# Optimization experiments

Measured on AMD Instinct MI355X. Metric: run time of the kernel, lower is better.

Reference implementation:

```python
import jax, jax.numpy as jnp
import numpy as np

B, S, E = 2, 4096, 640
H, D, G = 4, 256, 1      # n_heads, head_dim, n_kv_groups
WINDOW = 512
SCALING = 256.0 ** -0.5  # query_pre_attn_scalar ** -0.5
EPS = 1e-6


def rmsnorm(x, scale):
    # Gemma variant: weight = 1 + scale, computed in fp32 over last dim
    xf = x.astype(jnp.float32)
    var = jnp.mean(xf * xf, axis=-1, keepdims=True)
    return (xf * jax.lax.rsqrt(var + EPS) * (1.0 + scale.astype(jnp.float32))).astype(x.dtype)


def apply_rope(x, cos, sin):
    # x: [B, h, S, D]; cos/sin: [S, D]
    half = x.shape[-1] // 2
    x1, x2 = x[..., :half], x[..., half:]
    rotated = jnp.concatenate([-x2, x1], axis=-1)
    return (x * cos[None, None] + rotated * sin[None, None]).astype(x.dtype)


def setup_inputs() -> dict:
    key = jax.random.key(0)
    ks = jax.random.split(key, 6)
    x = jax.random.normal(ks[0], (B, S, E), dtype=jnp.float32)
    # weights (torch Linear weight.T layout: [in, out])
    Wq = jax.random.normal(ks[1], (E, H * D), dtype=jnp.float32) * 0.02
    Wk = jax.random.normal(ks[2], (E, G * D), dtype=jnp.float32) * 0.02
    Wv = jax.random.normal(ks[3], (E, G * D), dtype=jnp.float32) * 0.02
    Wo = jax.random.normal(ks[4], (H * D, E), dtype=jnp.float32) * 0.02
    q_scale = jnp.zeros((D,), dtype=jnp.float32)
    k_scale = jnp.zeros((D,), dtype=jnp.float32)
    # RoPE tables (theta = rope_local_base = 10000 for sliding layers)
    inv_freq = 1.0 / (10000.0 ** (jnp.arange(0, D, 2, dtype=jnp.float32) / D))
    angles = jnp.arange(S, dtype=jnp.float32)[:, None] * inv_freq[None, :]
    angles = jnp.concatenate([angles, angles], axis=1)  # [S, D]
    cos, sin = jnp.cos(angles), jnp.sin(angles)
    # causal + sliding-window mask; True = masked out
    i = jnp.arange(S)[:, None]
    j = jnp.arange(S)[None, :]
    mask = (j > i) | ((i - j) >= WINDOW)
    return {"x": x, "mask": mask, "cos": cos, "sin": sin,
            "Wq": Wq, "Wk": Wk, "Wv": Wv, "Wo": Wo,
            "q_scale": q_scale, "k_scale": k_scale}


def reference(x, mask, cos, sin, Wq, Wk, Wv, Wo, q_scale, k_scale):
    b, s, _ = x.shape
    q = (x @ Wq).reshape(b, s, H, D).transpose(0, 2, 1, 3)  # [B,H,S,D]
    k = (x @ Wk).reshape(b, s, G, D).transpose(0, 2, 1, 3)  # [B,G,S,D]
    v = (x @ Wv).reshape(b, s, G, D).transpose(0, 2, 1, 3)  # [B,G,S,D]
    q = rmsnorm(q, q_scale)
    k = rmsnorm(k, k_scale)
    q = apply_rope(q, cos, sin)
    k = apply_rope(k, cos, sin)
    # GQA: K/V have G=1 heads; broadcasting replaces repeat_interleave
    scores = (q * SCALING) @ jnp.swapaxes(k, -1, -2)  # [B,H,S,S]
    scores = jnp.where(mask[None, None], -jnp.inf, scores)
    attn = jax.nn.softmax(scores, axis=-1)
    out = attn @ v                                     # [B,H,S,D]
    out = out.transpose(0, 2, 1, 3).reshape(b, s, H * D)
    return out @ Wo
```

## Files before the change

kernel.cpp:

```cpp
#include <hip/hip_runtime.h>
#include <hip/hip_bf16.h>
#include <stdint.h>

#define BB 2
#define SS 4096
#define EE 640
#define HH 4
#define DD 256
#define WIN 512

typedef __attribute__((ext_vector_type(8))) short bv8;
typedef __attribute__((ext_vector_type(4))) float fv4;
typedef __attribute__((ext_vector_type(16))) float fv16;

__device__ __forceinline__ unsigned short f2b(float f) {
  union { float f; unsigned u; } a; a.f = f;
  unsigned r = a.u + 0x7fffu + ((a.u >> 16) & 1u);
  return (unsigned short)(r >> 16);
}
__device__ __forceinline__ float b2f(unsigned short s) {
  union { unsigned u; float f; } a; a.u = ((unsigned)s) << 16;
  return a.f;
}
__device__ __forceinline__ unsigned pk2(float lo, float hi_) {
  return (unsigned)f2b(lo) | ((unsigned)f2b(hi_) << 16);
}

typedef const __attribute__((address_space(1))) unsigned int* as1u;
typedef __attribute__((address_space(3))) unsigned int* as3u;
__device__ __forceinline__ void gld16(const unsigned short* g, unsigned short* l) {
  __builtin_amdgcn_global_load_lds((as1u)(const void*)g, (as3u)(void*)l, 16, 0, 0);
}

__global__ __launch_bounds__(256) void k_cast_bf16(const float* __restrict__ src,
                                                   unsigned short* __restrict__ dst, int n4) {
  int i = blockIdx.x * 256 + threadIdx.x;
  if (i >= n4) return;
  fv4 v = ((const fv4*)src)[i];
  ushort4 o; o.x = f2b(v.x); o.y = f2b(v.y); o.z = f2b(v.z); o.w = f2b(v.w);
  ((ushort4*)dst)[i] = o;
}

template <typename T>
__global__ __launch_bounds__(256) void k_transpose_bf16(const T* __restrict__ src,
    unsigned short* __restrict__ dst, int sstride, int dstride) {
  __shared__ float tile[32][33];
  int r0 = blockIdx.x * 32, c0 = blockIdx.y * 32;
  int t = threadIdx.x;
  int rr = t >> 3, cc = (t & 7) * 4;
  const T* p = src + (size_t)(r0 + rr) * sstride + c0 + cc;
  float v[4];
  if constexpr (sizeof(T) == 4) {
    fv4 x = *(const fv4*)p;
    v[0] = x.x; v[1] = x.y; v[2] = x.z; v[3] = x.w;
  } else {
    ushort4 x = *(const ushort4*)p;
    v[0] = b2f(x.x); v[1] = b2f(x.y); v[2] = b2f(x.z); v[3] = b2f(x.w);
  }
#pragma unroll
  for (int i = 0; i < 4; ++i) tile[cc + i][rr] = v[i];
  __syncthreads();
  ushort4 o;
  o.x = f2b(tile[rr][cc + 0]); o.y = f2b(tile[rr][cc + 1]);
  o.z = f2b(tile[rr][cc + 2]); o.w = f2b(tile[rr][cc + 3]);
  *(ushort4*)(dst + (size_t)(c0 + rr) * dstride + r0 + cc) = o;
}

template <bool OUT_BF16, int BN>
__global__ __launch_bounds__(256) void k_gemm(const unsigned short* __restrict__ A,
    const unsigned short* __restrict__ Bt, void* __restrict__ Cp,
    int M, int N, int K, int nt_n) {
  __shared__ unsigned short la[128 * 32];
  __shared__ unsigned short lb[BN * 32];
  const int bid = blockIdx.x;
  const int gidx = (bid & 7) * (gridDim.x >> 3) + (bid >> 3);
  const int m0 = (gidx / nt_n) * 128, n0 = (gidx % nt_n) * BN;
  const int tid = threadIdx.x, lane = tid & 63, wave = tid >> 6;
  const int g = lane >> 4, lr = lane & 15;
  constexpr int MI = (BN == 128) ? 4 : 2;
  const int wm = (BN == 128) ? (wave >> 1) * 64 : wave * 32;
  const int wn = (BN == 128) ? (wave & 1) * 64 : 0;
  fv4 acc[MI][4] = {};
  const int srow = wave * 32 + (lane >> 2);
  const int sch = (lane & 3) * 8;
  const unsigned short* ga0 = A + (size_t)(m0 + srow) * K + sch;
  unsigned short* lad = la + wave * 1024;
  const int srowb = (BN == 128) ? srow : (wave * 16 + (lane >> 2));
  const unsigned short* gb0 = Bt + (size_t)(n0 + srowb) * K + sch;
  unsigned short* lbd = lb + ((BN == 128) ? wave * 1024 : wave * 512);
  for (int k0 = 0; k0 < K; k0 += 32) {
    __syncthreads();
    gld16(ga0 + k0, lad);
    gld16(ga0 + (size_t)16 * K + k0, lad + 512);
    gld16(gb0 + k0, lbd);
    if constexpr (BN == 128) gld16(gb0 + (size_t)16 * K + k0, lbd + 512);
    __syncthreads();
    bv8 af[MI], bf[4];
#pragma unroll
    for (int mi = 0; mi < MI; ++mi) af[mi] = *(const bv8*)(la + (wm + mi * 16 + lr) * 32 + g * 8);
#pragma unroll
    for (int ni = 0; ni < 4; ++ni) bf[ni] = *(const bv8*)(lb + (wn + ni * 16 + lr) * 32 + g * 8);
    __builtin_amdgcn_s_setprio(1);
#pragma unroll
    for (int mi = 0; mi < MI; ++mi)
#pragma unroll
      for (int ni = 0; ni < 4; ++ni)
        acc[mi][ni] = __builtin_amdgcn_mfma_f32_16x16x32_bf16(af[mi], bf[ni], acc[mi][ni], 0, 0, 0);
    __builtin_amdgcn_s_setprio(0);
  }
#pragma unroll
  for (int mi = 0; mi < MI; ++mi) {
#pragma unroll
    for (int r = 0; r < 4; ++r) {
      size_t row = (size_t)(m0 + wm + mi * 16 + g * 4 + r);
#pragma unroll
      for (int ni = 0; ni < 4; ++ni) {
        int col = n0 + wn + ni * 16 + lr;
        float val = acc[mi][ni][r];
        if constexpr (OUT_BF16)
          ((unsigned short*)Cp)[row * N + col] = f2b(val);
        else
          ((float*)Cp)[row * N + col] = val;
      }
    }
  }
}

__global__ __launch_bounds__(320) void k_normrope(const unsigned short* __restrict__ qkv,
    const float* __restrict__ cosp, const float* __restrict__ sinp,
    const float* __restrict__ qsc, const float* __restrict__ ksc,
    unsigned short* __restrict__ qo, unsigned short* __restrict__ ko) {
  int m = blockIdx.x;
  int b = m >> 12, s = m & 4095;
  int wave = threadIdx.x >> 6, lane = threadIdx.x & 63;
  bool isq = wave < 4;
  const unsigned short* src = qkv + (size_t)m * 1536 + (isq ? wave * 256 : 1024);
  const float* scp = isq ? qsc : ksc;
  int d0 = lane * 4;
  ushort4 raw = *(const ushort4*)(src + d0);
  float x0 = b2f(raw.x), x1 = b2f(raw.y), x2 = b2f(raw.z), x3 = b2f(raw.w);
  float ss = x0 * x0 + x1 * x1 + x2 * x2 + x3 * x3;
#pragma unroll
  for (int off = 1; off < 64; off <<= 1) ss += __shfl_xor(ss, off, 64);
  float rs = rsqrtf(ss * (1.0f / 256.0f) + 1e-6f);
  fv4 sc = *(const fv4*)(scp + d0);
  float n0 = x0 * rs * (1.0f + sc.x);
  float n1 = x1 * rs * (1.0f + sc.y);
  float n2 = x2 * rs * (1.0f + sc.z);
  float n3 = x3 * rs * (1.0f + sc.w);
  float p0 = __shfl_xor(n0, 32, 64);
  float p1 = __shfl_xor(n1, 32, 64);
  float p2 = __shfl_xor(n2, 32, 64);
  float p3 = __shfl_xor(n3, 32, 64);
  float sgn = (lane < 32) ? -1.0f : 1.0f;
  fv4 c4 = *(const fv4*)(cosp + (size_t)s * 256 + d0);
  fv4 s4 = *(const fv4*)(sinp + (size_t)s * 256 + d0);
  float mult = isq ? (0.0625f * 1.44269504f) : 1.0f;
  float o0 = (n0 * c4.x + sgn * p0 * s4.x) * mult;
  float o1 = (n1 * c4.y + sgn * p1 * s4.y) * mult;
  float o2 = (n2 * c4.z + sgn * p2 * s4.z) * mult;
  float o3 = (n3 * c4.w + sgn * p3 * s4.w) * mult;
  ushort4 o; o.x = f2b(o0); o.y = f2b(o1); o.z = f2b(o2); o.w = f2b(o3);
  unsigned short* dst = isq
      ? qo + ((size_t)(b * HH + wave) * SS + s) * 256 + d0
      : ko + ((size_t)b * SS + s) * 256 + d0;
  *(ushort4*)dst = o;
}

__global__ __launch_bounds__(512, 2) void k_attn(const unsigned short* __restrict__ q,
    const unsigned short* __restrict__ kg, const unsigned short* __restrict__ vtg,
    unsigned short* __restrict__ att) {
  __shared__ __align__(16) char ldsbuf[133120];
  __shared__ float lsb[4][32];
  unsigned short* kt = (unsigned short*)ldsbuf;
  unsigned short* vl = (unsigned short*)ldsbuf + 32768;
  const int bid = blockIdx.x;
  const int gidx = (bid & 7) * 32 + (bid >> 3);
  const int b = gidx >> 7;
  const int i0 = (gidx & 127) * 32;
  const int tid = threadIdx.x, wave = tid >> 6, lane = tid & 63;
  const int h = wave >> 1, ks = wave & 1;
  const int hi = lane >> 5, l31 = lane & 31;
  bv8 qf[16];
  {
    const unsigned short* qp = q + ((size_t)(b * HH + h) * SS + i0 + l31) * 256;
#pragma unroll
    for (int m = 0; m < 16; ++m) qf[m] = *(const bv8*)(qp + m * 16 + hi * 8);
  }
  fv16 po[8] = {};
  float lsp = 0.f;
  const int t0 = (i0 >= WIN) ? ((i0 - WIN + 1) >> 6) : 0;
  const int t1 = i0 >> 6;
  const unsigned short* kb = kg + (size_t)b * SS * 256;
  const unsigned short* vb = vtg + (size_t)b * 256 * SS;
  auto stageK = [&](int t, int pp) {
    const unsigned short* kbase = kb + (size_t)t * 64 * 256;
    unsigned short* dst = kt + pp * 16384;
#pragma unroll
    for (int c = 0; c < 4; ++c) {
      int slot = c * 512 + tid;
      int row = slot >> 5, s = slot & 31;
      gld16(kbase + (size_t)row * 256 + ((s ^ (row & 7)) * 8),
            dst + (c * 512 + wave * 64) * 8);
    }
  };
  auto stageV = [&](int t, int pp) {
    const unsigned short* vbase = vb + (size_t)t * 64;
    unsigned short* dst = vl + pp * 16384;
#pragma unroll
    for (int c = 0; c < 4; ++c) {
      int slot = c * 512 + tid;
      int d_ = slot >> 3, s = slot & 7;
      gld16(vbase + (size_t)d_ * SS + ((s ^ (d_ & 7)) * 8),
            dst + (c * 512 + wave * 64) * 8);
    }
  };
  stageK(t0, 0); stageV(t0, 0);
  __syncthreads();
  int p = 0;
  const int krow = ks * 32 + l31;
  const int krx = krow & 7;
  const int vrx = l31 & 7;
  const float FSUB = 16.5f * 1.44269504f;
  for (int t = t0; t <= t1; ++t) {
    if (t > t0) __builtin_amdgcn_s_barrier();
    if (t < t1) {
      stageK(t + 1, p ^ 1); stageV(t + 1, p ^ 1);
      asm volatile("s_waitcnt vmcnt(8)" ::: "memory");
    } else {
      asm volatile("s_waitcnt vmcnt(0)" ::: "memory");
    }
    __builtin_amdgcn_sched_barrier(0);
    __builtin_amdgcn_s_barrier();
    fv16 sa = {};
    const unsigned short* ktp = kt + p * 16384 + krow * 256;
    __builtin_amdgcn_s_setprio(1);
#pragma unroll
    for (int m = 0; m < 16; ++m) {
      bv8 kf = *(const bv8*)(ktp + (((m * 2 + hi) ^ krx) * 8));
      sa = __builtin_amdgcn_mfma_f32_32x32x16_bf16(kf, qf[m], sa, 0, 0, 0);
    }
    __builtin_amdgcn_s_setprio(0);
    const int kb0 = t * 64 + ks * 32;
    const bool nm = (kb0 + 31 > i0) || (i0 + 31 - kb0 >= WIN);
    if (nm) {
      const int qa = i0 + l31;
#pragma unroll
      for (int r = 0; r < 16; ++r) {
        int j = kb0 + (r & 3) + 8 * (r >> 2) + 4 * hi;
        if (j > qa || qa - j >= WIN) sa[r] = -1e30f;
      }
    }
    unsigned a[8];
#pragma unroll
    for (int i = 0; i < 8; ++i) {
      float e0 = exp2f(sa[2 * i] - FSUB);
      float e1 = exp2f(sa[2 * i + 1] - FSUB);
      lsp += e0 + e1;
      a[i] = pk2(e0, e1);
    }
    const unsigned short* vlp = vl + p * 16384;
    __builtin_amdgcn_s_setprio(1);
#pragma unroll
    for (int m2 = 0; m2 < 2; ++m2) {
      auto r02 = __builtin_amdgcn_permlane32_swap(a[m2 * 4 + 0], a[m2 * 4 + 2], false, false);
      auto r13 = __builtin_amdgcn_permlane32_swap(a[m2 * 4 + 1], a[m2 * 4 + 3], false, false);
      union { unsigned u[4]; bv8 v; } pf;
      pf.u[0] = r02[0]; pf.u[1] = r13[0]; pf.u[2] = r02[1]; pf.u[3] = r13[1];
      const int slot = (ks * 4 + m2 * 2 + hi) ^ vrx;
#pragma unroll
      for (int ds_ = 0; ds_ < 8; ++ds_) {
        bv8 vf = *(const bv8*)(vlp + (ds_ * 32 + l31) * 64 + slot * 8);
        po[ds_] = __builtin_amdgcn_mfma_f32_32x32x16_bf16(vf, pf.v, po[ds_], 0, 0, 0);
      }
    }
    __builtin_amdgcn_s_setprio(0);
    p ^= 1;
  }
  float lsfull = lsp + __shfl_xor(lsp, 32, 64);
  __syncthreads();
  float* cb = (float*)ldsbuf;
  if (ks == 1) {
#pragma unroll
    for (int ds_ = 0; ds_ < 8; ++ds_)
#pragma unroll
      for (int j = 0; j < 4; ++j) {
        int d0 = ds_ * 32 + 8 * j + 4 * hi;
        fv4 v4; v4[0] = po[ds_][4 * j]; v4[1] = po[ds_][4 * j + 1];
        v4[2] = po[ds_][4 * j + 2]; v4[3] = po[ds_][4 * j + 3];
        *(fv4*)(cb + (h * 32 + l31) * 260 + d0) = v4;
      }
    if (lane < 32) lsb[h][lane] = lsfull;
  }
  __syncthreads();
  if (ks == 0) {
    float total = lsfull + lsb[h][l31];
    float inv = 1.0f / total;
    unsigned short* op = att + ((size_t)b * SS + i0 + l31) * 1024 + h * 256;
#pragma unroll
    for (int ds_ = 0; ds_ < 8; ++ds_)
#pragma unroll
      for (int j = 0; j < 4; ++j) {
        int d0 = ds_ * 32 + 8 * j + 4 * hi;
        fv4 v4 = *(const fv4*)(cb + (h * 32 + l31) * 260 + d0);
        ushort4 o;
        o.x = f2b((po[ds_][4 * j] + v4[0]) * inv);
        o.y = f2b((po[ds_][4 * j + 1] + v4[1]) * inv);
        o.z = f2b((po[ds_][4 * j + 2] + v4[2]) * inv);
        o.w = f2b((po[ds_][4 * j + 3] + v4[3]) * inv);
        *(ushort4*)(op + d0) = o;
      }
  }
}

extern "C" void kernel_launch(void* const* d_in, const int* in_sizes, int n_in,
                              void* d_out, int out_size, void* d_ws, size_t ws_size,
                              hipStream_t stream) {
  const float* x    = (const float*)d_in[0];
  const float* cosp = (const float*)d_in[2];
  const float* sinp = (const float*)d_in[3];
  const float* Wq   = (const float*)d_in[4];
  const float* Wk   = (const float*)d_in[5];
  const float* Wv   = (const float*)d_in[6];
  const float* Wo   = (const float*)d_in[7];
  const float* qsc  = (const float*)d_in[8];
  const float* ksc  = (const float*)d_in[9];
  float* out = (float*)d_out;
  char* ws = (char*)d_ws;

  unsigned short* xb   = (unsigned short*)(ws);
  unsigned short* wqkv = (unsigned short*)(ws + 10485760);
  unsigned short* wo   = (unsigned short*)(ws + 12451840);
  unsigned short* qkv  = (unsigned short*)(ws + 13762560);
  unsigned short* qb   = (unsigned short*)(ws + 38928384);
  unsigned short* kbuf = (unsigned short*)(ws + 55705600);
  unsigned short* vt   = (unsigned short*)(ws + 59899904);
  unsigned short* attb = (unsigned short*)(ws + 64094208);

  k_cast_bf16<<<5120, 256, 0, stream>>>(x, xb, 1310720);
  k_transpose_bf16<float><<<dim3(20, 32), 256, 0, stream>>>(Wq, wqkv, 1024, 640);
  k_transpose_bf16<float><<<dim3(20, 8), 256, 0, stream>>>(Wk, wqkv + 1024 * 640, 256, 640);
  k_transpose_bf16<float><<<dim3(20, 8), 256, 0, stream>>>(Wv, wqkv + 1280 * 640, 256, 640);
  k_transpose_bf16<float><<<dim3(32, 20), 256, 0, stream>>>(Wo, wo, 640, 1024);
  k_gemm<true, 128><<<768, 256, 0, stream>>>(xb, wqkv, qkv, 8192, 1536, 640, 12);
  k_normrope<<<8192, 320, 0, stream>>>(qkv, cosp, sinp, qsc, ksc, qb, kbuf);
  k_transpose_bf16<unsigned short><<<dim3(128, 8), 256, 0, stream>>>(qkv + 1280, vt, 1536, 4096);
  k_transpose_bf16<unsigned short><<<dim3(128, 8), 256, 0, stream>>>(
      qkv + (size_t)4096 * 1536 + 1280, vt + (size_t)256 * 4096, 1536, 4096);
  k_attn<<<256, 512, 0, stream>>>(qb, kbuf, vt, attb);
  k_gemm<false, 64><<<640, 256, 0, stream>>>(attb, wo, out, 8192, 640, 1024, 10);
}
```

Baseline: 124.5 us.

## Double-buffer GEMM LDS staging, merge transpose launches, simplify attention loop sync

Folds the four weight-transpose launches into one 3D-grid kernel and the two V-transpose launches into one, cutting launch overhead. The GEMM now double-buffers its LDS tiles and prefetches the next K-slice with partial vmcnt waits, overlapping global loads with MFMA work. The attention loop drops its explicit vmcnt/split-barrier prefetch scheduling in favour of a plain __syncthreads and stage-next. That may lose load/compute overlap, and without an explicit wait it may read K/V tiles whose async loads have not finished.

```diff
diff --git a/kernel.cpp b/kernel.cpp
--- a/kernel.cpp
+++ b/kernel.cpp
@@ -41,37 +41,55 @@
   ((ushort4*)dst)[i] = o;
 }
 
-template <typename T>
-__global__ __launch_bounds__(256) void k_transpose_bf16(const T* __restrict__ src,
-    unsigned short* __restrict__ dst, int sstride, int dstride) {
+__global__ __launch_bounds__(256) void k_wtrans(const float* __restrict__ Wq,
+    const float* __restrict__ Wk, const float* __restrict__ Wv,
+    const float* __restrict__ Wo, unsigned short* __restrict__ wqkv,
+    unsigned short* __restrict__ wo) {
   __shared__ float tile[32][33];
-  int r0 = blockIdx.x * 32, c0 = blockIdx.y * 32;
+  const int z = blockIdx.z, bx = blockIdx.x, by = blockIdx.y;
+  const float* src; unsigned short* dst; int ss, ds;
+  if (z == 0)      { if (bx >= 20 || by >= 32) return; src = Wq; dst = wqkv;              ss = 1024; ds = 640; }
+  else if (z == 1) { if (bx >= 20 || by >= 8)  return; src = Wk; dst = wqkv + 1024 * 640; ss = 256;  ds = 640; }
+  else if (z == 2) { if (bx >= 20 || by >= 8)  return; src = Wv; dst = wqkv + 1280 * 640; ss = 256;  ds = 640; }
+  else             { if (bx >= 32 || by >= 20) return; src = Wo; dst = wo;                ss = 640;  ds = 1024; }
+  int r0 = bx * 32, c0 = by * 32;
   int t = threadIdx.x;
   int rr = t >> 3, cc = (t & 7) * 4;
-  const T* p = src + (size_t)(r0 + rr) * sstride + c0 + cc;
-  float v[4];
-  if constexpr (sizeof(T) == 4) {
-    fv4 x = *(const fv4*)p;
-    v[0] = x.x; v[1] = x.y; v[2] = x.z; v[3] = x.w;
-  } else {
-    ushort4 x = *(const ushort4*)p;
-    v[0] = b2f(x.x); v[1] = b2f(x.y); v[2] = b2f(x.z); v[3] = b2f(x.w);
-  }
-#pragma unroll
-  for (int i = 0; i < 4; ++i) tile[cc + i][rr] = v[i];
+  fv4 x = *(const fv4*)(src + (size_t)(r0 + rr) * ss + c0 + cc);
+#pragma unroll
+  for (int i = 0; i < 4; ++i) tile[cc + i][rr] = x[i];
   __syncthreads();
   ushort4 o;
   o.x = f2b(tile[rr][cc + 0]); o.y = f2b(tile[rr][cc + 1]);
   o.z = f2b(tile[rr][cc + 2]); o.w = f2b(tile[rr][cc + 3]);
-  *(ushort4*)(dst + (size_t)(c0 + rr) * dstride + r0 + cc) = o;
+  *(ushort4*)(dst + (size_t)(c0 + rr) * ds + r0 + cc) = o;
+}
+
+__global__ __launch_bounds__(256) void k_vtrans(const unsigned short* __restrict__ qkv,
+    unsigned short* __restrict__ vt) {
+  __shared__ float tile[32][33];
+  const int z = blockIdx.z;
+  const unsigned short* src = qkv + (size_t)z * 4096 * 1536 + 1280;
+  unsigned short* dst = vt + (size_t)z * 256 * 4096;
+  int r0 = blockIdx.x * 32, c0 = blockIdx.y * 32;
+  int t = threadIdx.x;
+  int rr = t >> 3, cc = (t & 7) * 4;
+  ushort4 x = *(const ushort4*)(src + (size_t)(r0 + rr) * 1536 + c0 + cc);
+  tile[cc + 0][rr] = b2f(x.x); tile[cc + 1][rr] = b2f(x.y);
+  tile[cc + 2][rr] = b2f(x.z); tile[cc + 3][rr] = b2f(x.w);
+  __syncthreads();
+  ushort4 o;
+  o.x = f2b(tile[rr][cc + 0]); o.y = f2b(tile[rr][cc + 1]);
+  o.z = f2b(tile[rr][cc + 2]); o.w = f2b(tile[rr][cc + 3]);
+  *(ushort4*)(dst + (size_t)(c0 + rr) * 4096 + r0 + cc) = o;
 }
 
 template <bool OUT_BF16, int BN>
 __global__ __launch_bounds__(256) void k_gemm(const unsigned short* __restrict__ A,
     const unsigned short* __restrict__ Bt, void* __restrict__ Cp,
     int M, int N, int K, int nt_n) {
-  __shared__ unsigned short la[128 * 32];
-  __shared__ unsigned short lb[BN * 32];
+  __shared__ unsigned short la[2][128 * 32];
+  __shared__ unsigned short lb[2][BN * 32];
   const int bid = blockIdx.x;
   const int gidx = (bid & 7) * (gridDim.x >> 3) + (bid >> 3);
   const int m0 = (gidx / nt_n) * 128, n0 = (gidx % nt_n) * BN;
@@ -84,22 +102,39 @@
   const int srow = wave * 32 + (lane >> 2);
   const int sch = (lane & 3) * 8;
   const unsigned short* ga0 = A + (size_t)(m0 + srow) * K + sch;
-  unsigned short* lad = la + wave * 1024;
   const int srowb = (BN == 128) ? srow : (wave * 16 + (lane >> 2));
   const unsigned short* gb0 = Bt + (size_t)(n0 + srowb) * K + sch;
-  unsigned short* lbd = lb + ((BN == 128) ? wave * 1024 : wave * 512);
-  for (int k0 = 0; k0 < K; k0 += 32) {
-    __syncthreads();
+  const int NIT = K >> 5;
+  auto stage = [&](int k0, int pp) {
+    unsigned short* lad = la[pp] + wave * 1024;
+    unsigned short* lbd = lb[pp] + ((BN == 128) ? wave * 1024 : wave * 512);
     gld16(ga0 + k0, lad);
     gld16(ga0 + (size_t)16 * K + k0, lad + 512);
     gld16(gb0 + k0, lbd);
     if constexpr (BN == 128) gld16(gb0 + (size_t)16 * K + k0, lbd + 512);
-    __syncthreads();
+  };
+  stage(0, 0);
+  for (int it = 0; it < NIT; ++it) {
+    const int p = it & 1;
+    if (it > 0) __builtin_amdgcn_s_barrier();
+    if (it + 1 < NIT) {
+      stage((it + 1) * 32, p ^ 1);
+      if constexpr (BN == 128)
+        asm volatile("s_waitcnt vmcnt(4)" ::: "memory");
+      else
+        asm volatile("s_waitcnt vmcnt(3)" ::: "memory");
+    } else {
+      asm volatile("s_waitcnt vmcnt(0)" ::: "memory");
+    }
+    __builtin_amdgcn_sched_barrier(0);
+    __builtin_amdgcn_s_barrier();
     bv8 af[MI], bf[4];
 #pragma unroll
-    for (int mi = 0; mi < MI; ++mi) af[mi] = *(const bv8*)(la + (wm + mi * 16 + lr) * 32 + g * 8);
-#pragma unroll
-    for (int ni = 0; ni < 4; ++ni) bf[ni] = *(const bv8*)(lb + (wn + ni * 16 + lr) * 32 + g * 8);
+    for (int mi = 0; mi < MI; ++mi)
+      af[mi] = *(const bv8*)(la[p] + (wm + mi * 16 + lr) * 32 + g * 8);
+#pragma unroll
+    for (int ni = 0; ni < 4; ++ni)
+      bf[ni] = *(const bv8*)(lb[p] + (wn + ni * 16 + lr) * 32 + g * 8);
     __builtin_amdgcn_s_setprio(1);
 #pragma unroll
     for (int mi = 0; mi < MI; ++mi)
@@ -216,22 +251,14 @@
     }
   };
   stageK(t0, 0); stageV(t0, 0);
-  __syncthreads();
   int p = 0;
   const int krow = ks * 32 + l31;
   const int krx = krow & 7;
   const int vrx = l31 & 7;
   const float FSUB = 16.5f * 1.44269504f;
   for (int t = t0; t <= t1; ++t) {
-    if (t > t0) __builtin_amdgcn_s_barrier();
-    if (t < t1) {
-      stageK(t + 1, p ^ 1); stageV(t + 1, p ^ 1);
-      asm volatile("s_waitcnt vmcnt(8)" ::: "memory");
-    } else {
-      asm volatile("s_waitcnt vmcnt(0)" ::: "memory");
-    }
-    __builtin_amdgcn_sched_barrier(0);
-    __builtin_amdgcn_s_barrier();
+    __syncthreads();
+    if (t < t1) { stageK(t + 1, p ^ 1); stageV(t + 1, p ^ 1); }
     fv16 sa = {};
     const unsigned short* ktp = kt + p * 16384 + krow * 256;
     __builtin_amdgcn_s_setprio(1);
@@ -338,15 +365,10 @@
   unsigned short* attb = (unsigned short*)(ws + 64094208);
 
   k_cast_bf16<<<5120, 256, 0, stream>>>(x, xb, 1310720);
-  k_transpose_bf16<float><<<dim3(20, 32), 256, 0, stream>>>(Wq, wqkv, 1024, 640);
-  k_transpose_bf16<float><<<dim3(20, 8), 256, 0, stream>>>(Wk, wqkv + 1024 * 640, 256, 640);
-  k_transpose_bf16<float><<<dim3(20, 8), 256, 0, stream>>>(Wv, wqkv + 1280 * 640, 256, 640);
-  k_transpose_bf16<float><<<dim3(32, 20), 256, 0, stream>>>(Wo, wo, 640, 1024);
+  k_wtrans<<<dim3(32, 32, 4), 256, 0, stream>>>(Wq, Wk, Wv, Wo, wqkv, wo);
   k_gemm<true, 128><<<768, 256, 0, stream>>>(xb, wqkv, qkv, 8192, 1536, 640, 12);
   k_normrope<<<8192, 320, 0, stream>>>(qkv, cosp, sinp, qsc, ksc, qb, kbuf);
-  k_transpose_bf16<unsigned short><<<dim3(128, 8), 256, 0, stream>>>(qkv + 1280, vt, 1536, 4096);
-  k_transpose_bf16<unsigned short><<<dim3(128, 8), 256, 0, stream>>>(
-      qkv + (size_t)4096 * 1536 + 1280, vt + (size_t)256 * 4096, 1536, 4096);
+  k_vtrans<<<dim3(128, 8, 2), 256, 0, stream>>>(qkv, vt);
   k_attn<<<256, 512, 0, stream>>>(qb, kbuf, vt, attb);
   k_gemm<false, 64><<<640, 256, 0, stream>>>(attb, wo, out, 8192, 640, 1024, 10);
 }
```

Measured after the change: 115.0 us. 7.6% less time.
